# Optimization experiments

Measured on AMD Instinct MI355X. Metric: run time of the kernel, lower is better.

The kernel has to match this reference:

```python
import jax, jax.numpy as jnp
import numpy as np

N = 100_000      # nodes
E = 1_600_000    # edges (avg degree 16)
F_IN = 165       # Elliptic node features
HID = 64         # hidden_units
NCLS = 2         # num_classes
NEG_SLOPE = 0.2  # PyG GATConv default


def setup_inputs() -> dict:
    key = jax.random.key(0)
    ks = jax.random.split(key, 9)
    x = jax.random.normal(ks[0], (N, F_IN), jnp.float32)
    edge_index = jax.random.randint(ks[1], (2, E), 0, N, jnp.int32)
    W1 = jax.random.normal(ks[2], (F_IN, HID), jnp.float32) / np.sqrt(F_IN)
    a1_src = jax.random.normal(ks[3], (HID,), jnp.float32) / np.sqrt(HID)
    a1_dst = jax.random.normal(ks[4], (HID,), jnp.float32) / np.sqrt(HID)
    b1 = jnp.zeros((HID,), jnp.float32)
    W2 = jax.random.normal(ks[5], (HID, NCLS), jnp.float32) / np.sqrt(HID)
    a2_src = jax.random.normal(ks[6], (NCLS,), jnp.float32) / np.sqrt(NCLS)
    a2_dst = jax.random.normal(ks[7], (NCLS,), jnp.float32) / np.sqrt(NCLS)
    b2 = jnp.zeros((NCLS,), jnp.float32)
    return {"x": x, "edge_index": edge_index, "W1": W1, "a1_src": a1_src,
            "a1_dst": a1_dst, "b1": b1, "W2": W2, "a2_src": a2_src,
            "a2_dst": a2_dst, "b2": b2}


def gat_layer(x, src, dst, W, a_s, a_d, b, n):
    # h: [N, out]; per-edge attention e_ij = LeakyReLU(a_s.h_j + a_d.h_i)
    h = x @ W
    e = jax.nn.leaky_relu((h @ a_s)[src] + (h @ a_d)[dst], NEG_SLOPE)
    # numerically stable segment softmax over incoming edges of each dst node
    emax = jax.ops.segment_max(e, dst, num_segments=n)
    ee = jnp.exp(e - jax.lax.stop_gradient(emax)[dst])
    denom = jax.ops.segment_sum(ee, dst, num_segments=n)
    alpha = ee / denom[dst]                       # [E_tot]
    out = jax.ops.segment_sum(alpha[:, None] * h[src], dst, num_segments=n)
    return out + b


def reference(x, edge_index, W1, a1_src, a1_dst, b1, W2, a2_src, a2_dst, b2):
    n = x.shape[0]
    loops = jnp.arange(n, dtype=edge_index.dtype)   # PyG add_self_loops=True
    src = jnp.concatenate([edge_index[0], loops])
    dst = jnp.concatenate([edge_index[1], loops])
    h = jax.nn.relu(gat_layer(x, src, dst, W1, a1_src, a1_dst, b1, n))
    # F.dropout(training=False) is identity in eval mode
    out = gat_layer(h, src, dst, W2, a2_src, a2_dst, b2, n)
    return out, edge_index
```

## Files before the change

kernel.cpp:

```cpp
#include <hip/hip_runtime.h>
#include <hip/hip_bf16.h>
#include <math.h>

#define N_NODES 100000
#define N_EDGES 1600000
#define F_IN 165
#define HID 64
#define SLOPE 0.2f

#define NBUCK 196
#define BSHIFT 9
#define BMASK 511
#define NBLK 256
#define CHUNK 6250
#define MSCAN (NBUCK * NBLK)

typedef short short8 __attribute__((ext_vector_type(8)));
typedef float f32x4 __attribute__((ext_vector_type(4)));
typedef float f32x2 __attribute__((ext_vector_type(2)));

__device__ __forceinline__ float lrelu(float x) { return x > 0.f ? x : SLOPE * x; }

__device__ __forceinline__ unsigned short f2bf(float f) {
    unsigned u = __float_as_uint(f);
    u += 0x7FFFu + ((u >> 16) & 1u);
    return (unsigned short)(u >> 16);
}
__device__ __forceinline__ float bflo(unsigned u) { return __uint_as_float(u << 16); }
__device__ __forceinline__ float bfhi(unsigned u) { return __uint_as_float(u & 0xFFFF0000u); }
__device__ __forceinline__ unsigned char f2fp8(float f) {
    return (unsigned char)(__builtin_amdgcn_cvt_pk_fp8_f32(f, f, 0, false) & 0xFF);
}

__global__ __launch_bounds__(256) void k_hist(const int* __restrict__ ei,
                                              int* __restrict__ hist,
                                              float* __restrict__ out_edges,
                                              const float* __restrict__ W1,
                                              unsigned short* __restrict__ Wsw) {
    int blk = blockIdx.x, t = threadIdx.x;
    int idx = blk * 256 + t;
    if (idx < 12288) {
        int j = idx & 7;
        int r = idx >> 3;
        int n = r & 15; r >>= 4;
        int tt = r & 3; r >>= 2;
        int q = r & 3;  int c = r >> 2;
        int k = c * 32 + q * 8 + j;
        int col = tt * 16 + n;
        float v = (k < F_IN) ? W1[k * HID + col] : 0.f;
        Wsw[idx] = f2bf(v);
    }
    __shared__ int h[NBUCK];
    for (int j = t; j < NBUCK; j += 256) h[j] = 0;
    __syncthreads();
    int i0 = blk * CHUNK, i1 = i0 + CHUNK;
    for (int i = i0 + t * 2; i < i1; i += 512) {
        int2 sv = *(const int2*)&ei[i];
        int2 dv = *(const int2*)&ei[N_EDGES + i];
        *(float2*)&out_edges[i] = make_float2((float)sv.x, (float)sv.y);
        *(float2*)&out_edges[N_EDGES + i] = make_float2((float)dv.x, (float)dv.y);
        atomicAdd(&h[dv.x >> BSHIFT], 1);
        atomicAdd(&h[dv.y >> BSHIFT], 1);
    }
    __syncthreads();
    for (int j = t; j < NBUCK; j += 256) hist[j * NBLK + blk] = h[j];
}

#define ASTRIDE 200
__global__ __launch_bounds__(256, 4) void k_gemm1(const float* __restrict__ x,
                                                  const unsigned short* __restrict__ Wsw,
                                                  const float* __restrict__ a1s,
                                                  const float* __restrict__ a1d,
                                                  unsigned char* __restrict__ h1,
                                                  float* __restrict__ s1,
                                                  float* __restrict__ d1) {
    __shared__ unsigned short Ah[64 * ASTRIDE];
    const int tid = threadIdx.x;
    const int base = blockIdx.x * 64;
    const bool full = (base + 64 <= N_NODES);

    for (int i = tid; i < 64 * 35; i += 256) {
        int nl = i / 35, kk = 165 + (i - nl * 35);
        Ah[nl * ASTRIDE + kk] = 0;
    }
    const int fbase = base * F_IN;
    const int flim = N_NODES * F_IN;
    {
        int i4 = tid * 4;
        int nl = i4 / F_IN;
        int kk = i4 - nl * F_IN;
#pragma unroll
        for (int it = 0; it < 11; it++) {
            if (i4 < 64 * F_IN) {
                int f = fbase + i4;
                float vv[4];
                if (full || f + 4 <= flim) {
                    float4 v = *(const float4*)&x[f];
                    vv[0] = v.x; vv[1] = v.y; vv[2] = v.z; vv[3] = v.w;
                } else {
#pragma unroll
                    for (int e = 0; e < 4; e++) vv[e] = (f + e < flim) ? x[f + e] : 0.f;
                }
                int n0 = nl, k0 = kk;
#pragma unroll
                for (int e = 0; e < 4; e++) {
                    Ah[n0 * ASTRIDE + k0] = f2bf(vv[e]);
                    k0++;
                    if (k0 == F_IN) { k0 = 0; n0++; }
                }
            }
            i4 += 1024;
            nl += 6; kk += 34;
            if (kk >= F_IN) { kk -= F_IN; nl++; }
        }
    }
    __syncthreads();

    const int lane = tid & 63;
    const int w = tid >> 6;
    const int m16 = lane & 15;
    const int q = lane >> 4;
    f32x4 acc[4];
#pragma unroll
    for (int t = 0; t < 4; t++) acc[t] = (f32x4){0.f, 0.f, 0.f, 0.f};

    const unsigned short* arow = &Ah[(w * 16 + m16) * ASTRIDE];
    const short8* Wsw8 = (const short8*)Wsw;
#pragma unroll
    for (int c = 0; c < 6; c++) {
        short8 a = *(const short8*)&arow[c * 32 + q * 8];
#pragma unroll
        for (int t = 0; t < 4; t++) {
            short8 b = Wsw8[(c * 4 + q) * 64 + t * 16 + m16];
            acc[t] = __builtin_amdgcn_mfma_f32_16x16x32_bf16(a, b, acc[t], 0, 0, 0);
        }
    }

    float as_l[4], ad_l[4];
#pragma unroll
    for (int t = 0; t < 4; t++) { as_l[t] = a1s[t * 16 + m16]; ad_l[t] = a1d[t * 16 + m16]; }
#pragma unroll
    for (int r = 0; r < 4; r++) {
        int node = base + w * 16 + q * 4 + r;
        bool ok = node < N_NODES;
        float ps = 0.f, pd = 0.f;
#pragma unroll
        for (int t = 0; t < 4; t++) {
            float v = acc[t][r];
            if (ok) h1[(size_t)node * HID + t * 16 + m16] = f2fp8(v);
            ps += v * as_l[t];
            pd += v * ad_l[t];
        }
#pragma unroll
        for (int off = 1; off < 16; off <<= 1) {
            ps += __shfl_xor(ps, off);
            pd += __shfl_xor(pd, off);
        }
        if (ok && m16 == 0) { s1[node] = ps; d1[node] = pd; }
    }
}

__global__ void k_scan1(int* __restrict__ a, int* __restrict__ bsum) {
    __shared__ int sd[256];
    int i = blockIdx.x * 256 + threadIdx.x;
    int v = a[i];
    sd[threadIdx.x] = v;
    __syncthreads();
    for (int off = 1; off < 256; off <<= 1) {
        int t = (threadIdx.x >= off) ? sd[threadIdx.x - off] : 0;
        __syncthreads();
        sd[threadIdx.x] += t;
        __syncthreads();
    }
    a[i] = sd[threadIdx.x] - v;
    if (threadIdx.x == 255) bsum[blockIdx.x] = sd[255];
}

__global__ void k_scan2(int* __restrict__ bsum, int nb) {
    __shared__ int sd[256];
    int t = threadIdx.x;
    int v = (t < nb) ? bsum[t] : 0;
    sd[t] = v;
    __syncthreads();
    for (int off = 1; off < 256; off <<= 1) {
        int u = (t >= off) ? sd[t - off] : 0;
        __syncthreads();
        sd[t] += u;
        __syncthreads();
    }
    if (t < nb) bsum[t] = sd[t] - v;
}

__global__ __launch_bounds__(256) void k_part(const int* __restrict__ ei,
                                              const int* __restrict__ off,
                                              const int* __restrict__ bsum,
                                              unsigned* __restrict__ pairs) {
    __shared__ int base_s[NBUCK];
    __shared__ int cnt[NBUCK];
    int blk = blockIdx.x, t = threadIdx.x;
    for (int j = t; j < NBUCK; j += 256) {
        base_s[j] = off[j * NBLK + blk] + bsum[j];
        cnt[j] = 0;
    }
    __syncthreads();
    int i0 = blk * CHUNK, i1 = i0 + CHUNK;
    for (int i = i0 + t * 2; i < i1; i += 512) {
        int2 sv = *(const int2*)&ei[i];
        int2 dv = *(const int2*)&ei[N_EDGES + i];
        int b0 = dv.x >> BSHIFT;
        int p0 = base_s[b0] + atomicAdd(&cnt[b0], 1);
        pairs[p0] = ((unsigned)sv.x << BSHIFT) | (unsigned)(dv.x & BMASK);
        int b1v = dv.y >> BSHIFT;
        int p1 = base_s[b1v] + atomicAdd(&cnt[b1v], 1);
        pairs[p1] = ((unsigned)sv.y << BSHIFT) | (unsigned)(dv.y & BMASK);
    }
}

__global__ __launch_bounds__(512) void k_build2(const unsigned* __restrict__ pairs,
                                                const int* __restrict__ off,
                                                const int* __restrict__ bsum,
                                                int* __restrict__ row_ptr,
                                                int* __restrict__ deg,
                                                int* __restrict__ csr) {
    __shared__ int hcnt[512];
    __shared__ int cur[512];
    int b = blockIdx.x, t = threadIdx.x;
    hcnt[t] = 0;
    __syncthreads();
    int rs = off[b * NBLK] + bsum[b];
    int re = (b == NBUCK - 1) ? N_EDGES : off[(b + 1) * NBLK] + bsum[b + 1];
    for (int j = rs + t; j < re; j += 512)
        atomicAdd(&hcnt[pairs[j] & BMASK], 1);
    __syncthreads();
    int v = hcnt[t];
    cur[t] = v;
    __syncthreads();
    for (int o = 1; o < 512; o <<= 1) {
        int u = (t >= o) ? cur[t - o] : 0;
        __syncthreads();
        cur[t] += u;
        __syncthreads();
    }
    int excl = cur[t] - v;
    __syncthreads();
    cur[t] = rs + excl;
    int node = b * 512 + t;
    if (node < N_NODES) {
        row_ptr[node] = rs + excl;
        deg[node] = v;
    }
    __syncthreads();
    for (int j = rs + t; j < re; j += 512) {
        unsigned p = pairs[j];
        int pos = atomicAdd(&cur[p & BMASK], 1);
        csr[pos] = (int)(p >> BSHIFT);
    }
}

__global__ __launch_bounds__(256, 8) void k_agg1(const unsigned char* __restrict__ h1,
                                                 const float* __restrict__ s1,
                                                 const float* __restrict__ d1,
                                                 const int* __restrict__ row_ptr,
                                                 const int* __restrict__ deg,
                                                 const int* __restrict__ csr,
                                                 const float* __restrict__ b1,
                                                 const float* __restrict__ W2,
                                                 const float* __restrict__ a2s,
                                                 const float* __restrict__ a2d,
                                                 uint2* __restrict__ node2,
                                                 float* __restrict__ d2arr) {
    int gwid = (blockIdx.x * blockDim.x + threadIdx.x) >> 6;
    int lane = threadIdx.x & 63;
    int node = gwid * 4 + (lane >> 4);
    int cg = lane & 15;
    if (node >= N_NODES) return;
    float di = d1[node];
    int rs = row_ptr[node], re = rs + deg[node];
    float dpart = 0.f;
    float4 acc = make_float4(0.f, 0.f, 0.f, 0.f);
    const unsigned char* hb = h1 + cg * 4;

    for (int j0 = rs; j0 < re; j0 += 8) {
        int sv[8]; float ev[8];
#pragma unroll
        for (int k = 0; k < 8; k++) {
            int jk = j0 + k;
            int jc = jk < re ? jk : (re - 1);
            sv[k] = csr[jc];
            float e = __expf(lrelu(s1[sv[k]] + di));
            ev[k] = (jk < re) ? e : 0.f;
        }
        unsigned uv[8];
#pragma unroll
        for (int k = 0; k < 8; k++)
            uv[k] = *(const unsigned*)&hb[(size_t)sv[k] << 6];
#pragma unroll
        for (int k = 0; k < 8; k++) {
            f32x2 lo = __builtin_amdgcn_cvt_pk_f32_fp8((int)uv[k], false);
            f32x2 hi = __builtin_amdgcn_cvt_pk_f32_fp8((int)uv[k], true);
            dpart += ev[k];
            acc.x += ev[k] * lo.x; acc.y += ev[k] * lo.y;
            acc.z += ev[k] * hi.x; acc.w += ev[k] * hi.y;
        }
    }

    float ees = __expf(lrelu(s1[node] + di));
    unsigned us = *(const unsigned*)&hb[(size_t)node << 6];
    f32x2 slo = __builtin_amdgcn_cvt_pk_f32_fp8((int)us, false);
    f32x2 shi = __builtin_amdgcn_cvt_pk_f32_fp8((int)us, true);
    float denom = dpart + ees;
    acc.x += ees * slo.x; acc.y += ees * slo.y;
    acc.z += ees * shi.x; acc.w += ees * shi.y;
    float inv = 1.f / denom;
    float4 bb = *(const float4*)&b1[cg * 4];
    float o0 = fmaxf(acc.x * inv + bb.x, 0.f);
    float o1 = fmaxf(acc.y * inv + bb.y, 0.f);
    float o2 = fmaxf(acc.z * inv + bb.z, 0.f);
    float o3 = fmaxf(acc.w * inv + bb.w, 0.f);
    float2 w0 = *(const float2*)&W2[(cg * 4 + 0) * 2];
    float2 w1 = *(const float2*)&W2[(cg * 4 + 1) * 2];
    float2 w2 = *(const float2*)&W2[(cg * 4 + 2) * 2];
    float2 w3 = *(const float2*)&W2[(cg * 4 + 3) * 2];
    float p0 = o0 * w0.x + o1 * w1.x + o2 * w2.x + o3 * w3.x;
    float p1 = o0 * w0.y + o1 * w1.y + o2 * w2.y + o3 * w3.y;
#pragma unroll
    for (int off = 1; off < 16; off <<= 1) {
        p0 += __shfl_xor(p0, off);
        p1 += __shfl_xor(p1, off);
    }
    if (cg == 0) {
        float s2 = p0 * a2s[0] + p1 * a2s[1];
        float d2v = p0 * a2d[0] + p1 * a2d[1];
        unsigned pk = (unsigned)f2bf(p0) | ((unsigned)f2bf(p1) << 16);
        node2[node] = make_uint2(pk, __float_as_uint(s2));
        d2arr[node] = d2v;
    }
}

__global__ __launch_bounds__(256, 8) void k_agg2(const uint2* __restrict__ node2,
                                                 const float* __restrict__ d2arr,
                                                 const int* __restrict__ row_ptr,
                                                 const int* __restrict__ deg,
                                                 const int* __restrict__ csr,
                                                 const float* __restrict__ b2,
                                                 float* __restrict__ out) {
    int wid = (blockIdx.x * blockDim.x + threadIdx.x) >> 6;
    int lane = threadIdx.x & 63;
    int node = wid * 8 + (lane >> 3);
    int eg = lane & 7;
    if (node >= N_NODES) return;
    uint2 vi = node2[node];
    float d2 = d2arr[node];
    float denom = 0.f, p0 = 0.f, p1 = 0.f;
    int rs = row_ptr[node], re = rs + deg[node];
    for (int j = rs + eg; j < re; j += 16) {
        int j2 = j + 8;
        int j2c = j2 < re ? j2 : (re - 1);
        int sa = csr[j];
        int sb = csr[j2c];
        uint2 va = node2[sa];
        uint2 vb = node2[sb];
        float ea = __expf(lrelu(__uint_as_float(va.y) + d2));
        float eb = __expf(lrelu(__uint_as_float(vb.y) + d2));
        if (j2 >= re) eb = 0.f;
        denom += ea + eb;
        p0 += ea * bflo(va.x) + eb * bflo(vb.x);
        p1 += ea * bfhi(va.x) + eb * bfhi(vb.x);
    }
#pragma unroll
    for (int off = 1; off < 8; off <<= 1) {
        denom += __shfl_xor(denom, off);
        p0 += __shfl_xor(p0, off);
        p1 += __shfl_xor(p1, off);
    }
    if (eg == 0) {
        float ee = __expf(lrelu(__uint_as_float(vi.y) + d2));
        denom += ee;
        p0 += ee * bflo(vi.x);
        p1 += ee * bfhi(vi.x);
        out[(size_t)node * 2 + 0] = p0 / denom + b2[0];
        out[(size_t)node * 2 + 1] = p1 / denom + b2[1];
    }
}

extern "C" void kernel_launch(void* const* d_in, const int* in_sizes, int n_in,
                              void* d_out, int out_size, void* d_ws, size_t ws_size,
                              hipStream_t stream) {
    const float* x   = (const float*)d_in[0];
    const int*   ei  = (const int*)d_in[1];
    const float* W1  = (const float*)d_in[2];
    const float* a1s = (const float*)d_in[3];
    const float* a1d = (const float*)d_in[4];
    const float* b1  = (const float*)d_in[5];
    const float* W2  = (const float*)d_in[6];
    const float* a2s = (const float*)d_in[7];
    const float* a2d = (const float*)d_in[8];
    const float* b2  = (const float*)d_in[9];
    float* out = (float*)d_out;

    unsigned char* h1 = (unsigned char*)d_ws;
    float* s1      = (float*)(h1 + (size_t)N_NODES * HID);
    float* d1      = s1 + N_NODES;
    float* d2arr   = d1 + N_NODES;
    uint2* node2   = (uint2*)(d2arr + N_NODES);
    int* row_ptr   = (int*)(node2 + N_NODES);
    int* deg       = row_ptr + N_NODES;
    int* off       = deg + N_NODES;
    int* bsum      = off + MSCAN + 64;
    int* csr       = bsum + 256;
    unsigned* pairs = (unsigned*)(csr + N_EDGES);
    unsigned short* Wsw = (unsigned short*)(pairs + N_EDGES);

    k_hist<<<NBLK, 256, 0, stream>>>(ei, off, out + 2 * N_NODES, W1, Wsw);
    k_gemm1<<<(N_NODES + 63) / 64, 256, 0, stream>>>(x, Wsw, a1s, a1d, h1, s1, d1);
    k_scan1<<<MSCAN / 256, 256, 0, stream>>>(off, bsum);
    k_scan2<<<1, 256, 0, stream>>>(bsum, MSCAN / 256);
    k_part<<<NBLK, 256, 0, stream>>>(ei, off, bsum, pairs);
    k_build2<<<NBUCK, 512, 0, stream>>>(pairs, off, bsum, row_ptr, deg, csr);
    k_agg1<<<(N_NODES + 15) / 16, 256, 0, stream>>>(h1, s1, d1, row_ptr, deg, csr,
                                                    b1, W2, a2s, a2d, node2, d2arr);
    k_agg2<<<(N_NODES + 31) / 32, 256, 0, stream>>>(node2, d2arr, row_ptr, deg, csr, b2, out);
}
```

Baseline: 209.7 us.

## Split layer-1 aggregation into channel halves and merge with atomics

Layer-1 aggregation now runs each node in two blocks, each covering 32 of the 64 channels with 8 lanes per node. Consecutive blocks in a group process the same half, so each block gathers a smaller slice of h1, which may improve cache locality. Partial layer-2 projections are combined with float atomics into a zero-initialised float2 buffer, and agg2 computes the attention scores from them on the fly. The edge-index float copy moves from k_hist to k_part, which already reads the source indices. The cost is twice the edge traversal and exp work in agg1, an extra memset, atomic traffic, and fp32 gathers in agg2 instead of packed bf16.

```diff
diff --git a/kernel.cpp b/kernel.cpp
--- a/kernel.cpp
+++ b/kernel.cpp
@@ -14,6 +14,7 @@
 #define NBLK 256
 #define CHUNK 6250
 #define MSCAN (NBUCK * NBLK)
+#define NGRP 3125
 
 typedef short short8 __attribute__((ext_vector_type(8)));
 typedef float f32x4 __attribute__((ext_vector_type(4)));
@@ -26,15 +27,12 @@
     u += 0x7FFFu + ((u >> 16) & 1u);
     return (unsigned short)(u >> 16);
 }
-__device__ __forceinline__ float bflo(unsigned u) { return __uint_as_float(u << 16); }
-__device__ __forceinline__ float bfhi(unsigned u) { return __uint_as_float(u & 0xFFFF0000u); }
 __device__ __forceinline__ unsigned char f2fp8(float f) {
     return (unsigned char)(__builtin_amdgcn_cvt_pk_fp8_f32(f, f, 0, false) & 0xFF);
 }
 
 __global__ __launch_bounds__(256) void k_hist(const int* __restrict__ ei,
                                               int* __restrict__ hist,
-                                              float* __restrict__ out_edges,
                                               const float* __restrict__ W1,
                                               unsigned short* __restrict__ Wsw) {
     int blk = blockIdx.x, t = threadIdx.x;
@@ -55,10 +53,7 @@
     __syncthreads();
     int i0 = blk * CHUNK, i1 = i0 + CHUNK;
     for (int i = i0 + t * 2; i < i1; i += 512) {
-        int2 sv = *(const int2*)&ei[i];
         int2 dv = *(const int2*)&ei[N_EDGES + i];
-        *(float2*)&out_edges[i] = make_float2((float)sv.x, (float)sv.y);
-        *(float2*)&out_edges[N_EDGES + i] = make_float2((float)dv.x, (float)dv.y);
         atomicAdd(&h[dv.x >> BSHIFT], 1);
         atomicAdd(&h[dv.y >> BSHIFT], 1);
     }
@@ -194,7 +189,8 @@
 __global__ __launch_bounds__(256) void k_part(const int* __restrict__ ei,
                                               const int* __restrict__ off,
                                               const int* __restrict__ bsum,
-                                              unsigned* __restrict__ pairs) {
+                                              unsigned* __restrict__ pairs,
+                                              float* __restrict__ out_edges) {
     __shared__ int base_s[NBUCK];
     __shared__ int cnt[NBUCK];
     int blk = blockIdx.x, t = threadIdx.x;
@@ -207,6 +203,8 @@
     for (int i = i0 + t * 2; i < i1; i += 512) {
         int2 sv = *(const int2*)&ei[i];
         int2 dv = *(const int2*)&ei[N_EDGES + i];
+        *(float2*)&out_edges[i] = make_float2((float)sv.x, (float)sv.y);
+        *(float2*)&out_edges[N_EDGES + i] = make_float2((float)dv.x, (float)dv.y);
         int b0 = dv.x >> BSHIFT;
         int p0 = base_s[b0] + atomicAdd(&cnt[b0], 1);
         pairs[p0] = ((unsigned)sv.x << BSHIFT) | (unsigned)(dv.x & BMASK);
@@ -265,20 +263,22 @@
                                                  const int* __restrict__ csr,
                                                  const float* __restrict__ b1,
                                                  const float* __restrict__ W2,
-                                                 const float* __restrict__ a2s,
-                                                 const float* __restrict__ a2d,
-                                                 uint2* __restrict__ node2,
-                                                 float* __restrict__ d2arr) {
-    int gwid = (blockIdx.x * blockDim.x + threadIdx.x) >> 6;
+                                                 float2* __restrict__ node2p) {
+    int blk = blockIdx.x;
+    int j8 = blk & 7;
+    int half = j8 >> 2;
+    int ng = (blk >> 3) * 4 + (j8 & 3);
+    if (ng >= NGRP) return;
     int lane = threadIdx.x & 63;
-    int node = gwid * 4 + (lane >> 4);
-    int cg = lane & 15;
-    if (node >= N_NODES) return;
+    int w = threadIdx.x >> 6;
+    int node = ng * 32 + w * 8 + (lane >> 3);
+    int cg = lane & 7;
+    int ch0 = half * 32 + cg * 4;
     float di = d1[node];
     int rs = row_ptr[node], re = rs + deg[node];
     float dpart = 0.f;
     float4 acc = make_float4(0.f, 0.f, 0.f, 0.f);
-    const unsigned char* hb = h1 + cg * 4;
+    const unsigned char* hb = h1 + ch0;
 
     for (int j0 = rs; j0 < re; j0 += 8) {
         int sv[8]; float ev[8];
@@ -312,36 +312,34 @@
     acc.x += ees * slo.x; acc.y += ees * slo.y;
     acc.z += ees * shi.x; acc.w += ees * shi.y;
     float inv = 1.f / denom;
-    float4 bb = *(const float4*)&b1[cg * 4];
+    float4 bb = *(const float4*)&b1[ch0];
     float o0 = fmaxf(acc.x * inv + bb.x, 0.f);
     float o1 = fmaxf(acc.y * inv + bb.y, 0.f);
     float o2 = fmaxf(acc.z * inv + bb.z, 0.f);
     float o3 = fmaxf(acc.w * inv + bb.w, 0.f);
-    float2 w0 = *(const float2*)&W2[(cg * 4 + 0) * 2];
-    float2 w1 = *(const float2*)&W2[(cg * 4 + 1) * 2];
-    float2 w2 = *(const float2*)&W2[(cg * 4 + 2) * 2];
-    float2 w3 = *(const float2*)&W2[(cg * 4 + 3) * 2];
+    float2 w0 = *(const float2*)&W2[(ch0 + 0) * 2];
+    float2 w1 = *(const float2*)&W2[(ch0 + 1) * 2];
+    float2 w2 = *(const float2*)&W2[(ch0 + 2) * 2];
+    float2 w3 = *(const float2*)&W2[(ch0 + 3) * 2];
     float p0 = o0 * w0.x + o1 * w1.x + o2 * w2.x + o3 * w3.x;
     float p1 = o0 * w0.y + o1 * w1.y + o2 * w2.y + o3 * w3.y;
 #pragma unroll
-    for (int off = 1; off < 16; off <<= 1) {
+    for (int off = 1; off < 8; off <<= 1) {
         p0 += __shfl_xor(p0, off);
         p1 += __shfl_xor(p1, off);
     }
     if (cg == 0) {
-        float s2 = p0 * a2s[0] + p1 * a2s[1];
-        float d2v = p0 * a2d[0] + p1 * a2d[1];
-        unsigned pk = (unsigned)f2bf(p0) | ((unsigned)f2bf(p1) << 16);
-        node2[node] = make_uint2(pk, __float_as_uint(s2));
-        d2arr[node] = d2v;
-    }
-}
-
-__global__ __launch_bounds__(256, 8) void k_agg2(const uint2* __restrict__ node2,
-                                                 const float* __restrict__ d2arr,
+        atomicAdd(&node2p[node].x, p0);
+        atomicAdd(&node2p[node].y, p1);
+    }
+}
+
+__global__ __launch_bounds__(256, 8) void k_agg2(const float2* __restrict__ node2p,
                                                  const int* __restrict__ row_ptr,
                                                  const int* __restrict__ deg,
                                                  const int* __restrict__ csr,
+                                                 const float* __restrict__ a2s,
+                                                 const float* __restrict__ a2d,
                                                  const float* __restrict__ b2,
                                                  float* __restrict__ out) {
     int wid = (blockIdx.x * blockDim.x + threadIdx.x) >> 6;
@@ -349,8 +347,9 @@
     int node = wid * 8 + (lane >> 3);
     int eg = lane & 7;
     if (node >= N_NODES) return;
-    uint2 vi = node2[node];
-    float d2 = d2arr[node];
+    float s0 = a2s[0], s1c = a2s[1];
+    float2 vi = node2p[node];
+    float d2 = vi.x * a2d[0] + vi.y * a2d[1];
     float denom = 0.f, p0 = 0.f, p1 = 0.f;
     int rs = row_ptr[node], re = rs + deg[node];
     for (int j = rs + eg; j < re; j += 16) {
@@ -358,14 +357,14 @@
         int j2c = j2 < re ? j2 : (re - 1);
         int sa = csr[j];
         int sb = csr[j2c];
-        uint2 va = node2[sa];
-        uint2 vb = node2[sb];
-        float ea = __expf(lrelu(__uint_as_float(va.y) + d2));
-        float eb = __expf(lrelu(__uint_as_float(vb.y) + d2));
+        float2 va = node2p[sa];
+        float2 vb = node2p[sb];
+        float ea = __expf(lrelu(va.x * s0 + va.y * s1c + d2));
+        float eb = __expf(lrelu(vb.x * s0 + vb.y * s1c + d2));
         if (j2 >= re) eb = 0.f;
         denom += ea + eb;
-        p0 += ea * bflo(va.x) + eb * bflo(vb.x);
-        p1 += ea * bfhi(va.x) + eb * bfhi(vb.x);
+        p0 += ea * va.x + eb * vb.x;
+        p1 += ea * va.y + eb * vb.y;
     }
 #pragma unroll
     for (int off = 1; off < 8; off <<= 1) {
@@ -374,10 +373,10 @@
         p1 += __shfl_xor(p1, off);
     }
     if (eg == 0) {
-        float ee = __expf(lrelu(__uint_as_float(vi.y) + d2));
+        float ee = __expf(lrelu(vi.x * s0 + vi.y * s1c + d2));
         denom += ee;
-        p0 += ee * bflo(vi.x);
-        p1 += ee * bfhi(vi.x);
+        p0 += ee * vi.x;
+        p1 += ee * vi.y;
         out[(size_t)node * 2 + 0] = p0 / denom + b2[0];
         out[(size_t)node * 2 + 1] = p1 / denom + b2[1];
     }
@@ -401,9 +400,8 @@
     unsigned char* h1 = (unsigned char*)d_ws;
     float* s1      = (float*)(h1 + (size_t)N_NODES * HID);
     float* d1      = s1 + N_NODES;
-    float* d2arr   = d1 + N_NODES;
-    uint2* node2   = (uint2*)(d2arr + N_NODES);
-    int* row_ptr   = (int*)(node2 + N_NODES);
+    float2* node2p = (float2*)(d1 + N_NODES);
+    int* row_ptr   = (int*)(node2p + N_NODES);
     int* deg       = row_ptr + N_NODES;
     int* off       = deg + N_NODES;
     int* bsum      = off + MSCAN + 64;
@@ -411,13 +409,15 @@
     unsigned* pairs = (unsigned*)(csr + N_EDGES);
     unsigned short* Wsw = (unsigned short*)(pairs + N_EDGES);
 
-    k_hist<<<NBLK, 256, 0, stream>>>(ei, off, out + 2 * N_NODES, W1, Wsw);
+    k_hist<<<NBLK, 256, 0, stream>>>(ei, off, W1, Wsw);
     k_gemm1<<<(N_NODES + 63) / 64, 256, 0, stream>>>(x, Wsw, a1s, a1d, h1, s1, d1);
     k_scan1<<<MSCAN / 256, 256, 0, stream>>>(off, bsum);
     k_scan2<<<1, 256, 0, stream>>>(bsum, MSCAN / 256);
-    k_part<<<NBLK, 256, 0, stream>>>(ei, off, bsum, pairs);
+    k_part<<<NBLK, 256, 0, stream>>>(ei, off, bsum, pairs, out + 2 * N_NODES);
     k_build2<<<NBUCK, 512, 0, stream>>>(pairs, off, bsum, row_ptr, deg, csr);
-    k_agg1<<<(N_NODES + 15) / 16, 256, 0, stream>>>(h1, s1, d1, row_ptr, deg, csr,
-                                                    b1, W2, a2s, a2d, node2, d2arr);
-    k_agg2<<<(N_NODES + 31) / 32, 256, 0, stream>>>(node2, d2arr, row_ptr, deg, csr, b2, out);
-}
+    hipMemsetAsync(node2p, 0, (size_t)N_NODES * sizeof(float2), stream);
+    k_agg1<<<((NGRP + 3) / 4) * 8, 256, 0, stream>>>(h1, s1, d1, row_ptr, deg, csr,
+                                                     b1, W2, node2p);
+    k_agg2<<<(N_NODES + 31) / 32, 256, 0, stream>>>(node2p, row_ptr, deg, csr,
+                                                    a2s, a2d, b2, out);
+}
```

After: 235.7 us. 1.12x slower.
